# Optimization experiments

Hardware: AMD Instinct MI355X
Metric: run time of the kernel (lower is better)

The kernel has to match this reference:

```python
import jax, jax.numpy as jnp
import numpy as np

N_NODES = 50000
N_EDGES = 800000
N_GRAPHS = 512
D = 128
NUM_LAYERS = 3
BN_EPS = 1e-5


def setup_inputs() -> dict:
    key = jax.random.key(0)
    ks = jax.random.split(key, 16)
    x = jax.random.normal(ks[0], (N_NODES, D), dtype=jnp.float32)
    edge_index = jax.random.randint(ks[1], (2, N_EDGES), 0, N_NODES, dtype=jnp.int64)
    batch = jnp.sort(jax.random.randint(ks[2], (N_NODES,), 0, N_GRAPHS, dtype=jnp.int64))
    # per-layer MLP params (all dims are 128 so we can stack across layers)
    s1 = 1.0 / np.sqrt(D)
    W1 = jax.random.uniform(ks[3], (NUM_LAYERS, D, D), jnp.float32, -s1, s1)
    b1 = jax.random.uniform(ks[4], (NUM_LAYERS, D), jnp.float32, -s1, s1)
    W2 = jax.random.uniform(ks[5], (NUM_LAYERS, D, D), jnp.float32, -s1, s1)
    b2 = jax.random.uniform(ks[6], (NUM_LAYERS, D), jnp.float32, -s1, s1)
    eps = jnp.zeros((NUM_LAYERS,), jnp.float32)  # train_eps=True, init 0.0
    gamma = jnp.ones((NUM_LAYERS, D), jnp.float32)
    beta = jnp.zeros((NUM_LAYERS, D), jnp.float32)
    return {"x": x, "edge_index": edge_index, "batch": batch,
            "W1": W1, "b1": b1, "W2": W2, "b2": b2,
            "eps": eps, "gamma": gamma, "beta": beta}


def _gin_forward(x, edge_index, batch, W1, b1, W2, b2, eps, gamma, beta):
    src, dst = edge_index[0], edge_index[1]
    h = x
    for i in range(NUM_LAYERS):
        # GINConv: MLP((1+eps)*h_i + sum_{j->i} h_j)  (scatter-add over edges)
        agg = jax.ops.segment_sum(h[src], dst, num_segments=N_NODES)
        z = (1.0 + eps[i]) * h + agg
        z = jax.nn.relu(z @ W1[i] + b1[i]) @ W2[i] + b2[i]
        # BatchNorm1d (training-mode batch stats, biased variance)
        mean = jnp.mean(z, axis=0)
        var = jnp.mean(jnp.square(z - mean), axis=0)
        h = (z - mean) * jax.lax.rsqrt(var + BN_EPS) * gamma[i] + beta[i]
        if i < NUM_LAYERS - 1:
            h = jax.nn.relu(h)  # dropout is identity in eval mode
    # global_mean_pool over batch segment ids
    sums = jax.ops.segment_sum(h, batch, num_segments=N_GRAPHS)
    counts = jax.ops.segment_sum(jnp.ones((N_NODES, 1), h.dtype), batch, num_segments=N_GRAPHS)
    return sums / jnp.maximum(counts, 1.0)


def reference(x, edge_index, batch, W1, b1, W2, b2, eps, gamma, beta):
    return _gin_forward(x, edge_index, batch, W1, b1, W2, b2, eps, gamma, beta)
```

## Files before the change

kernel.cpp:

```cpp
#include <hip/hip_runtime.h>

#define N_NODESC 50000
#define N_EDGESC 800000
#define N_GRAPHSC 512
#define DF 128
#define BN_EPSF 1e-5f
#define CSR_CAP 64
#define CUR_STRIDE 32
#define LAYER_BLOCKS 3125
#define NSLICE 32
#define POISON 0xAAAAAAAAu

#define PREP_SCAT_B 3125
#define PREP_CONVX_B 3125
#define PREP_CONVW_B 48
#define PREP_ZERO_B 6
#define PREP_TOTAL_B (PREP_SCAT_B + PREP_CONVX_B + PREP_CONVW_B + PREP_ZERO_B)

typedef _Float16 half8 __attribute__((ext_vector_type(8)));
typedef _Float16 half2v __attribute__((ext_vector_type(2)));
typedef float floatx4 __attribute__((ext_vector_type(4)));

__global__ __launch_bounds__(256) void k_prep(
    const int* __restrict__ src, const int* __restrict__ dst,
    unsigned* __restrict__ cursor, unsigned short* __restrict__ csr,
    const float* __restrict__ x, _Float16* __restrict__ h,
    const float* __restrict__ W1, const float* __restrict__ W2, half8* __restrict__ wf,
    float* __restrict__ pb2)
{
    int b = blockIdx.x;
    int tid = threadIdx.x;
    if (b < PREP_SCAT_B) {
        int e = b * 256 + tid;
        int d = dst[e];
        int sv = src[e];
        unsigned pos = atomicAdd(&cursor[(size_t)d * CUR_STRIDE], 1u) - POISON;
        if (pos < CSR_CAP) csr[d * CSR_CAP + pos] = (unsigned short)sv;
    } else if (b < PREP_SCAT_B + PREP_CONVX_B) {
        int i8 = (b - PREP_SCAT_B) * 256 + tid;
        const floatx4* x4 = (const floatx4*)x;
        floatx4 v0 = __builtin_nontemporal_load(&x4[i8 * 2]);
        floatx4 v1 = __builtin_nontemporal_load(&x4[i8 * 2 + 1]);
        half8 o;
        o[0] = (_Float16)v0[0]; o[1] = (_Float16)v0[1]; o[2] = (_Float16)v0[2]; o[3] = (_Float16)v0[3];
        o[4] = (_Float16)v1[0]; o[5] = (_Float16)v1[1]; o[6] = (_Float16)v1[2]; o[7] = (_Float16)v1[3];
        ((half8*)h)[i8] = o;
    } else if (b < PREP_SCAT_B + PREP_CONVX_B + PREP_CONVW_B) {
        int t = (b - PREP_SCAT_B - PREP_CONVX_B) * 256 + tid;
        int m = t >> 11;
        int p = t & 2047;
        int ntile = p >> 8;
        int ks = (p >> 6) & 3;
        int l = p & 63;
        int n = ntile * 16 + (l & 15);
        int kb = ks * 32 + (l >> 4) * 8;
        const float* W = (m < 3) ? (W1 + (size_t)m * DF * DF) : (W2 + (size_t)(m - 3) * DF * DF);
        half8 o;
#pragma unroll
        for (int j = 0; j < 8; j++) o[j] = (_Float16)W[(size_t)(kb + j) * DF + n];
        wf[t] = o;
    } else {
        int b2 = b - (PREP_SCAT_B + PREP_CONVX_B + PREP_CONVW_B);
        floatx4* p4 = (floatx4*)pb2;
        int base = (b2 * 256 + tid) * 4;
#pragma unroll
        for (int j = 0; j < 4; j++) p4[base + j] = (floatx4)(0.f);
    }
}

#define TSTRIDE 136
template <int MODE>
__global__ __launch_bounds__(1024) void k_layer(
    const _Float16* __restrict__ Hin, const unsigned* __restrict__ cursor,
    const unsigned short* __restrict__ csr,
    const float* __restrict__ epsArr, int layer,
    const float* __restrict__ pbPrev, const float* __restrict__ gprev, const float* __restrict__ bprev,
    const half8* __restrict__ W1f, const float* __restrict__ b1,
    const half8* __restrict__ W2f, const float* __restrict__ b2,
    _Float16* __restrict__ Z, float* __restrict__ pbOut)
{
    __shared__ _Float16 At[16 * TSTRIDE];
    __shared__ _Float16 Bt[16 * TSTRIDE];
    __shared__ float red[4][256];
    __shared__ float scof[DF], ofof[DF];
    const int tid = threadIdx.x;
    const int w = tid >> 6, lane = tid & 63;

    if (MODE == 1) {
        int cc = tid & 255, sg = tid >> 8;
        float s = 0.f;
#pragma unroll
        for (int sl = 0; sl < 8; sl++) s += pbPrev[(sg + sl * 4) * 256 + cc];
        red[sg][cc] = s;
        __syncthreads();
        if (tid < 128) {
            const float invN = 1.f / (float)N_NODESC;
            float su = red[0][tid] + red[1][tid] + red[2][tid] + red[3][tid];
            float sq = red[0][128 + tid] + red[1][128 + tid] + red[2][128 + tid] + red[3][128 + tid];
            float m = su * invN;
            float var = sq * invN - m * m;
            float sc = gprev[tid] * rsqrtf(var + BN_EPSF);
            scof[tid] = sc;
            ofof[tid] = bprev[tid] - m * sc;
        }
        __syncthreads();
    }

    {
        int n = blockIdx.x * 16 + w;
        int g = lane >> 4, c16 = lane & 15;
        float sc[8], of[8];
        if (MODE == 1) {
#pragma unroll
            for (int i = 0; i < 8; i++) {
                sc[i] = scof[c16 * 8 + i];
                of[i] = ofof[c16 * 8 + i];
            }
        }
        const half8* Hr8 = (const half8*)Hin;
        int myidx = (int)csr[n * CSR_CAP + lane];
        int deg = (int)(cursor[(size_t)n * CUR_STRIDE] - POISON);
        if (deg > CSR_CAP) deg = CSR_CAP;

        float a[8];
#pragma unroll
        for (int i = 0; i < 8; i++) a[i] = 0.f;
        if (g == 0) {
            half8 u = Hr8[(size_t)n * 16 + c16];
            float e1 = 1.0f + epsArr[layer];
#pragma unroll
            for (int i = 0; i < 8; i++) {
                float xv = (float)u[i];
                if (MODE == 1) xv = fmaxf(xv * sc[i] + of[i], 0.f);
                a[i] = e1 * xv;
            }
        }
        int T = (deg + 7) >> 3;
        int k = g;
        for (int t = 0; t < T; t++, k += 8) {
            int m0 = __shfl(myidx, k);
            int m1 = __shfl(myidx, k + 4);
            bool ok0 = k < deg, ok1 = (k + 4) < deg;
            int mm0 = ok0 ? m0 : n;
            int mm1 = ok1 ? m1 : n;
            half8 u0 = Hr8[(size_t)mm0 * 16 + c16];
            half8 u1 = Hr8[(size_t)mm1 * 16 + c16];
            float f0 = ok0 ? 1.f : 0.f, f1 = ok1 ? 1.f : 0.f;
#pragma unroll
            for (int i = 0; i < 8; i++) {
                float x0 = (float)u0[i], x1 = (float)u1[i];
                if (MODE == 1) {
                    x0 = fmaxf(x0 * sc[i] + of[i], 0.f);
                    x1 = fmaxf(x1 * sc[i] + of[i], 0.f);
                }
                a[i] = fmaf(f0, x0, a[i]);
                a[i] = fmaf(f1, x1, a[i]);
            }
        }
#pragma unroll
        for (int i = 0; i < 8; i++) {
            a[i] += __shfl_xor(a[i], 16);
            a[i] += __shfl_xor(a[i], 32);
        }
        if (g == 0) {
            half8 o;
#pragma unroll
            for (int i = 0; i < 8; i++) o[i] = (_Float16)a[i];
            *(half8*)&At[w * TSTRIDE + c16 * 8] = o;
        }
    }
    __syncthreads();

    const int q = lane >> 4, c = lane & 15;
    if (w < 8) {
        half8 af[4];
#pragma unroll
        for (int ks = 0; ks < 4; ks++)
            af[ks] = *(const half8*)&At[c * TSTRIDE + ks * 32 + q * 8];
        floatx4 acc = (floatx4)(0.0f);
#pragma unroll
        for (int ks = 0; ks < 4; ks++) {
            half8 wfr = W1f[(w * 4 + ks) * 64 + lane];
            acc = __builtin_amdgcn_mfma_f32_16x16x32_f16(af[ks], wfr, acc, 0, 0, 0);
        }
        float b = b1[w * 16 + c];
#pragma unroll
        for (int r = 0; r < 4; r++) {
            float vv = fmaxf(acc[r] + b, 0.f);
            Bt[(q * 4 + r) * TSTRIDE + w * 16 + c] = (_Float16)vv;
        }
    }
    __syncthreads();

    if (w < 8) {
        half8 bf[4];
#pragma unroll
        for (int ks = 0; ks < 4; ks++)
            bf[ks] = *(const half8*)&Bt[c * TSTRIDE + ks * 32 + q * 8];
        floatx4 acc2 = (floatx4)(0.0f);
#pragma unroll
        for (int ks = 0; ks < 4; ks++) {
            half8 wfr = W2f[(w * 4 + ks) * 64 + lane];
            acc2 = __builtin_amdgcn_mfma_f32_16x16x32_f16(bf[ks], wfr, acc2, 0, 0, 0);
        }
        float b = b2[w * 16 + c];
        float ls = 0.f, lq = 0.f;
#pragma unroll
        for (int r = 0; r < 4; r++) {
            float vv = acc2[r] + b;
            ls += vv;
            lq += vv * vv;
            At[(q * 4 + r) * TSTRIDE + w * 16 + c] = (_Float16)vv;
        }
        ls += __shfl_xor(ls, 16);
        ls += __shfl_xor(ls, 32);
        lq += __shfl_xor(lq, 16);
        lq += __shfl_xor(lq, 32);
        if (q == 0) {
            float* pbb = pbOut + (size_t)(blockIdx.x & (NSLICE - 1)) * 256;
            atomicAdd(&pbb[w * 16 + c], ls);
            atomicAdd(&pbb[128 + w * 16 + c], lq);
        }
    }
    __syncthreads();

    half2v vz = *(const half2v*)&At[w * TSTRIDE + 2 * lane];
    ((half2v*)Z)[(size_t)(blockIdx.x * 16 + w) * 64 + lane] = vz;
}

static __device__ int lbound(const int* __restrict__ a, int n, int key) {
    int lo = 0, hi = n;
    while (lo < hi) {
        int mid = (lo + hi) >> 1;
        if (a[mid] < key) lo = mid + 1; else hi = mid;
    }
    return lo;
}

__global__ __launch_bounds__(128) void k_pool(const _Float16* __restrict__ Z, const int* __restrict__ batch,
                                              const float* __restrict__ pbL2, const float* __restrict__ gamma,
                                              const float* __restrict__ beta, float* __restrict__ out) {
    __shared__ int bnds[2];
    int g = blockIdx.x, c = threadIdx.x;
    if (threadIdx.x == 0) {
        bnds[0] = lbound(batch, N_NODESC, g);
        bnds[1] = lbound(batch, N_NODESC, g + 1);
    }
    float su = 0.f, sq = 0.f;
#pragma unroll 8
    for (int sl = 0; sl < NSLICE; sl++) {
        su += pbL2[sl * 256 + c];
        sq += pbL2[sl * 256 + 128 + c];
    }
    __syncthreads();
    const float invN = 1.f / (float)N_NODESC;
    float m = su * invN;
    float v = sq * invN - m * m;
    float sc = gamma[c] * rsqrtf(v + BN_EPSF);
    float of = beta[c] - m * sc;
    int lo = bnds[0], hi = bnds[1];
    float s = 0.f;
    int r = lo;
    for (; r + 4 <= hi; r += 4) {
        s += (float)Z[(size_t)r * DF + c] + (float)Z[(size_t)(r + 1) * DF + c]
           + (float)Z[(size_t)(r + 2) * DF + c] + (float)Z[(size_t)(r + 3) * DF + c];
    }
    for (; r < hi; r++) s += (float)Z[(size_t)r * DF + c];
    int cnt = hi - lo;
    out[g * DF + c] = (cnt > 0) ? (s / (float)cnt) * sc + of : 0.f;
}

extern "C" void kernel_launch(void* const* d_in, const int* in_sizes, int n_in,
                              void* d_out, int out_size, void* d_ws, size_t ws_size,
                              hipStream_t stream) {
    const float* x     = (const float*)d_in[0];
    const int*   ei    = (const int*)d_in[1];
    const int*   batch = (const int*)d_in[2];
    const float* W1    = (const float*)d_in[3];
    const float* b1    = (const float*)d_in[4];
    const float* W2    = (const float*)d_in[5];
    const float* b2    = (const float*)d_in[6];
    const float* eps   = (const float*)d_in[7];
    const float* gamma = (const float*)d_in[8];
    const float* beta  = (const float*)d_in[9];
    float* out = (float*)d_out;

    char* ws = (char*)d_ws;
    size_t o = 0;
    auto alloc = [&](size_t bytes) -> char* {
        char* p = ws + o;
        o += (bytes + 255) & ~(size_t)255;
        return p;
    };
    unsigned* cursor = (unsigned*)alloc((size_t)N_NODESC * CUR_STRIDE * sizeof(unsigned));
    unsigned short* csr = (unsigned short*)alloc((size_t)N_NODESC * CSR_CAP * sizeof(unsigned short));
    float* pb2     = (float*)alloc((size_t)3 * NSLICE * 256 * sizeof(float));
    half8* wf      = (half8*)alloc((size_t)6 * 2048 * sizeof(half8));
    _Float16* za   = (_Float16*)alloc((size_t)N_NODESC * DF * sizeof(_Float16));
    _Float16* zb   = (_Float16*)alloc((size_t)N_NODESC * DF * sizeof(_Float16));
    _Float16* hbuf = zb;
    (void)ws_size; (void)in_sizes; (void)n_in; (void)out_size;

    const int* srcA = ei;
    const int* dstA = ei + N_EDGESC;

    k_prep<<<PREP_TOTAL_B, 256, 0, stream>>>(srcA, dstA, cursor, csr, x, hbuf, W1, W2, wf, pb2);

    k_layer<0><<<LAYER_BLOCKS, 1024, 0, stream>>>(
        hbuf, cursor, csr, eps, 0, nullptr, nullptr, nullptr,
        wf + 0 * 2048, b1 + 0 * DF, wf + 3 * 2048, b2 + 0 * DF, za, pb2 + 0 * 8192);
    k_layer<1><<<LAYER_BLOCKS, 1024, 0, stream>>>(
        za, cursor, csr, eps, 1, pb2 + 0 * 8192, gamma + 0 * DF, beta + 0 * DF,
        wf + 1 * 2048, b1 + 1 * DF, wf + 4 * 2048, b2 + 1 * DF, zb, pb2 + 1 * 8192);
    k_layer<1><<<LAYER_BLOCKS, 1024, 0, stream>>>(
        zb, cursor, csr, eps, 2, pb2 + 1 * 8192, gamma + 1 * DF, beta + 1 * DF,
        wf + 2 * 2048, b1 + 2 * DF, wf + 5 * 2048, b2 + 2 * DF, za, pb2 + 2 * 8192);
    k_pool<<<N_GRAPHSC, DF, 0, stream>>>(za, batch, pb2 + 2 * 8192, gamma + 2 * DF, beta + 2 * DF, out);
}
```

Before: 269.6 us.

## Split BatchNorm+ReLU into standalone pass and widen gather unroll to four rows

The BN stats reduction and per-neighbor normalize+ReLU are moved out of the layer kernel into a separate in-place k_bn kernel that normalizes the whole Z buffer once. The gather loop then reads already-normalized rows and issues four independent neighbor loads per iteration instead of two. This removes the redundant per-edge scale/offset/ReLU arithmetic (about 16 reads per node) and the per-block stats reduction. In exchange it adds an extra kernel launch and a full read+write pass over the activations per layer, plus higher register pressure from the wider unroll.

After: 275.6 us. 1.02x slower.

```diff
diff --git a/kernel.cpp b/kernel.cpp
--- a/kernel.cpp
+++ b/kernel.cpp
@@ -68,55 +68,64 @@
     }
 }
 
+#define KBN_BLOCKS 256
+__global__ __launch_bounds__(256) void k_bn(
+    const float* __restrict__ pb, const float* __restrict__ gma, const float* __restrict__ bta,
+    _Float16* __restrict__ zh)
+{
+    __shared__ float red2[256];
+    __shared__ float scs[256];
+    int tid = threadIdx.x;
+    float s = 0.f;
+#pragma unroll
+    for (int sl = 0; sl < NSLICE; sl++) s += pb[sl * 256 + tid];
+    red2[tid] = s;
+    __syncthreads();
+    if (tid < 128) {
+        const float invN = 1.f / (float)N_NODESC;
+        float m = red2[tid] * invN;
+        float var = red2[128 + tid] * invN - m * m;
+        float sc = gma[tid] * rsqrtf(var + BN_EPSF);
+        scs[tid] = sc;
+        scs[128 + tid] = bta[tid] - m * sc;
+    }
+    __syncthreads();
+    int i0 = blockIdx.x * 256 + tid;
+    int cb = (i0 & 15) * 8;
+    float sc[8], of[8];
+#pragma unroll
+    for (int j = 0; j < 8; j++) { sc[j] = scs[cb + j]; of[j] = scs[128 + cb + j]; }
+    half8* z8 = (half8*)zh;
+    const int nch = N_NODESC * 16;
+    for (int i = i0; i < nch; i += KBN_BLOCKS * 256) {
+        half8 v = z8[i];
+        half8 o;
+#pragma unroll
+        for (int j = 0; j < 8; j++) {
+            float f = fmaf((float)v[j], sc[j], of[j]);
+            o[j] = (_Float16)fmaxf(f, 0.f);
+        }
+        z8[i] = o;
+    }
+}
+
 #define TSTRIDE 136
-template <int MODE>
 __global__ __launch_bounds__(1024) void k_layer(
     const _Float16* __restrict__ Hin, const unsigned* __restrict__ cursor,
     const unsigned short* __restrict__ csr,
     const float* __restrict__ epsArr, int layer,
-    const float* __restrict__ pbPrev, const float* __restrict__ gprev, const float* __restrict__ bprev,
     const half8* __restrict__ W1f, const float* __restrict__ b1,
     const half8* __restrict__ W2f, const float* __restrict__ b2,
     _Float16* __restrict__ Z, float* __restrict__ pbOut)
 {
     __shared__ _Float16 At[16 * TSTRIDE];
     __shared__ _Float16 Bt[16 * TSTRIDE];
-    __shared__ float red[4][256];
-    __shared__ float scof[DF], ofof[DF];
     const int tid = threadIdx.x;
     const int w = tid >> 6, lane = tid & 63;
-
-    if (MODE == 1) {
-        int cc = tid & 255, sg = tid >> 8;
-        float s = 0.f;
-#pragma unroll
-        for (int sl = 0; sl < 8; sl++) s += pbPrev[(sg + sl * 4) * 256 + cc];
-        red[sg][cc] = s;
-        __syncthreads();
-        if (tid < 128) {
-            const float invN = 1.f / (float)N_NODESC;
-            float su = red[0][tid] + red[1][tid] + red[2][tid] + red[3][tid];
-            float sq = red[0][128 + tid] + red[1][128 + tid] + red[2][128 + tid] + red[3][128 + tid];
-            float m = su * invN;
-            float var = sq * invN - m * m;
-            float sc = gprev[tid] * rsqrtf(var + BN_EPSF);
-            scof[tid] = sc;
-            ofof[tid] = bprev[tid] - m * sc;
-        }
-        __syncthreads();
-    }
 
     {
         int n = blockIdx.x * 16 + w;
         int g = lane >> 4, c16 = lane & 15;
-        float sc[8], of[8];
-        if (MODE == 1) {
-#pragma unroll
-            for (int i = 0; i < 8; i++) {
-                sc[i] = scof[c16 * 8 + i];
-                of[i] = ofof[c16 * 8 + i];
-            }
-        }
         const half8* Hr8 = (const half8*)Hin;
         int myidx = (int)csr[n * CSR_CAP + lane];
         int deg = (int)(cursor[(size_t)n * CUR_STRIDE] - POISON);
@@ -129,32 +138,28 @@
             half8 u = Hr8[(size_t)n * 16 + c16];
             float e1 = 1.0f + epsArr[layer];
 #pragma unroll
-            for (int i = 0; i < 8; i++) {
-                float xv = (float)u[i];
-                if (MODE == 1) xv = fmaxf(xv * sc[i] + of[i], 0.f);
-                a[i] = e1 * xv;
-            }
-        }
-        int T = (deg + 7) >> 3;
+            for (int i = 0; i < 8; i++) a[i] = e1 * (float)u[i];
+        }
+        int T = (deg + 15) >> 4;
         int k = g;
-        for (int t = 0; t < T; t++, k += 8) {
+        for (int t = 0; t < T; t++, k += 16) {
             int m0 = __shfl(myidx, k);
             int m1 = __shfl(myidx, k + 4);
-            bool ok0 = k < deg, ok1 = (k + 4) < deg;
-            int mm0 = ok0 ? m0 : n;
-            int mm1 = ok1 ? m1 : n;
-            half8 u0 = Hr8[(size_t)mm0 * 16 + c16];
-            half8 u1 = Hr8[(size_t)mm1 * 16 + c16];
+            int m2 = __shfl(myidx, k + 8);
+            int m3 = __shfl(myidx, k + 12);
+            bool ok0 = k < deg, ok1 = (k + 4) < deg, ok2 = (k + 8) < deg, ok3 = (k + 12) < deg;
+            half8 u0 = Hr8[(size_t)(ok0 ? m0 : n) * 16 + c16];
+            half8 u1 = Hr8[(size_t)(ok1 ? m1 : n) * 16 + c16];
+            half8 u2 = Hr8[(size_t)(ok2 ? m2 : n) * 16 + c16];
+            half8 u3 = Hr8[(size_t)(ok3 ? m3 : n) * 16 + c16];
             float f0 = ok0 ? 1.f : 0.f, f1 = ok1 ? 1.f : 0.f;
+            float f2 = ok2 ? 1.f : 0.f, f3 = ok3 ? 1.f : 0.f;
 #pragma unroll
             for (int i = 0; i < 8; i++) {
-                float x0 = (float)u0[i], x1 = (float)u1[i];
-                if (MODE == 1) {
-                    x0 = fmaxf(x0 * sc[i] + of[i], 0.f);
-                    x1 = fmaxf(x1 * sc[i] + of[i], 0.f);
-                }
-                a[i] = fmaf(f0, x0, a[i]);
-                a[i] = fmaf(f1, x1, a[i]);
+                a[i] = fmaf((float)u0[i], f0, a[i]);
+                a[i] = fmaf((float)u1[i], f1, a[i]);
+                a[i] = fmaf((float)u2[i], f2, a[i]);
+                a[i] = fmaf((float)u3[i], f3, a[i]);
             }
         }
 #pragma unroll
@@ -306,14 +311,16 @@
 
     k_prep<<<PREP_TOTAL_B, 256, 0, stream>>>(srcA, dstA, cursor, csr, x, hbuf, W1, W2, wf, pb2);
 
-    k_layer<0><<<LAYER_BLOCKS, 1024, 0, stream>>>(
-        hbuf, cursor, csr, eps, 0, nullptr, nullptr, nullptr,
+    k_layer<<<LAYER_BLOCKS, 1024, 0, stream>>>(
+        hbuf, cursor, csr, eps, 0,
         wf + 0 * 2048, b1 + 0 * DF, wf + 3 * 2048, b2 + 0 * DF, za, pb2 + 0 * 8192);
-    k_layer<1><<<LAYER_BLOCKS, 1024, 0, stream>>>(
-        za, cursor, csr, eps, 1, pb2 + 0 * 8192, gamma + 0 * DF, beta + 0 * DF,
+    k_bn<<<KBN_BLOCKS, 256, 0, stream>>>(pb2 + 0 * 8192, gamma + 0 * DF, beta + 0 * DF, za);
+    k_layer<<<LAYER_BLOCKS, 1024, 0, stream>>>(
+        za, cursor, csr, eps, 1,
         wf + 1 * 2048, b1 + 1 * DF, wf + 4 * 2048, b2 + 1 * DF, zb, pb2 + 1 * 8192);
-    k_layer<1><<<LAYER_BLOCKS, 1024, 0, stream>>>(
-        zb, cursor, csr, eps, 2, pb2 + 1 * 8192, gamma + 1 * DF, beta + 1 * DF,
+    k_bn<<<KBN_BLOCKS, 256, 0, stream>>>(pb2 + 1 * 8192, gamma + 1 * DF, beta + 1 * DF, zb);
+    k_layer<<<LAYER_BLOCKS, 1024, 0, stream>>>(
+        zb, cursor, csr, eps, 2,
         wf + 2 * 2048, b1 + 2 * DF, wf + 5 * 2048, b2 + 2 * DF, za, pb2 + 2 * 8192);
     k_pool<<<N_GRAPHSC, DF, 0, stream>>>(za, batch, pb2 + 2 * 8192, gamma + 2 * DF, beta + 2 * DF, out);
 }
```
